# Kernel tuning notes

Measured on AMD Instinct MI355X. Metric: run time of the kernel, lower is better.

The kernel has to match this reference:

```python
import jax, jax.numpy as jnp
import numpy as np

D = 512
H = 8
DH = D // H  # 64


def setup_inputs() -> dict:
    key = jax.random.key(0)
    ks = jax.random.split(key, 7)
    batch, la, lb = 8, 256, 256
    A = jax.random.normal(ks[0], (batch, la, D), dtype=jnp.float32)
    B = jax.random.normal(ks[1], (batch, lb, D), dtype=jnp.float32)
    s = 1.0 / np.sqrt(D)
    W1 = jax.random.uniform(ks[2], (D, D), minval=-s, maxval=s, dtype=jnp.float32)
    b1 = jax.random.uniform(ks[3], (D,), minval=-s, maxval=s, dtype=jnp.float32)
    W2 = jax.random.uniform(ks[4], (D, D), minval=-s, maxval=s, dtype=jnp.float32)
    b2 = jax.random.uniform(ks[5], (D,), minval=-s, maxval=s, dtype=jnp.float32)
    q = jax.random.normal(ks[6], (DH,), dtype=jnp.float32) * 0.1
    return {"A": A, "B": B, "W1": W1, "b1": b1, "W2": W2, "b2": b2, "q": q}


def reference(A, B, W1, b1, W2, b2, q):
    bs, la, _ = A.shape
    lb = B.shape[1]
    # Linear + ReLU, then raw row-major reshape to (batch, heads, len, dh)
    # (matches torch .view semantics: NOT a head-transpose split)
    A_ = jax.nn.relu(A @ W1.T + b1).reshape(bs, H, la, DH)
    B_ = jax.nn.relu(B @ W2.T + b2).reshape(bs, H, lb, DH)
    # bilinear score: tanh of elementwise pairwise product, dotted with q
    # att_maps: [bs, H, la, lb]
    att_maps = jnp.einsum(
        "bhijc,c->bhij",
        jnp.tanh(A_[:, :, :, None, :] * B_[:, :, None, :, :]),
        q,
    )
    temp_b2a = jax.nn.softmax(jnp.mean(att_maps, axis=3), axis=2)  # [bs,H,la]
    temp_a2b = jax.nn.softmax(jnp.mean(att_maps, axis=2), axis=2)  # [bs,H,lb]
    A_heads = A.reshape(bs, H, la, DH)
    B_heads = B.reshape(bs, H, lb, DH)
    A_p = jnp.sum(A_heads * temp_b2a[..., None], axis=2).reshape(bs, -1)  # [bs, d]
    B_p = jnp.sum(B_heads * temp_a2b[..., None], axis=2).reshape(bs, -1)  # [bs, d]
    return (
        jnp.concatenate((A_p, B_p), axis=1),
        jnp.mean(temp_b2a, axis=1),
        jnp.mean(temp_a2b, axis=1),
    )
```

## Files before the change

### kernel.cpp

```cpp
#include <hip/hip_runtime.h>
#include <hip/hip_bf16.h>

#define LOG2E 1.4426950408889634f
#define SC2   2.8853900817779268f

typedef __attribute__((ext_vector_type(8))) short short8b;
typedef __attribute__((ext_vector_type(4))) short short4b;
typedef __attribute__((ext_vector_type(4))) float f32x4;

__device__ __forceinline__ float fast_exp2(float x) {
#if __has_builtin(__builtin_amdgcn_exp2f)
  return __builtin_amdgcn_exp2f(x);
#else
  return exp2f(x);
#endif
}
__device__ __forceinline__ float fast_rcp(float x) {
#if __has_builtin(__builtin_amdgcn_rcpf)
  return __builtin_amdgcn_rcpf(x);
#else
  return 1.0f / x;
#endif
}
__device__ __forceinline__ short f2bf(float f) {
  __hip_bfloat16 h = __float2bfloat16(f);
  return *reinterpret_cast<short*>(&h);
}

__global__ __launch_bounds__(256) void gemm_mfma_kernel(
    const float* __restrict__ Xa, const float* __restrict__ Wa,
    const float* __restrict__ ba, float* __restrict__ Oa,
    const float* __restrict__ Xb, const float* __restrict__ Wb,
    const float* __restrict__ bb, float* __restrict__ Ob) {
  const float* X = blockIdx.z ? Xb : Xa;
  const float* W = blockIdx.z ? Wb : Wa;
  const float* bias = blockIdx.z ? bb : ba;
  float* O = blockIdx.z ? Ob : Oa;

  __shared__ __align__(16) short As[64 * 40];
  __shared__ __align__(16) short Ws[64 * 40];

  int t = threadIdx.x;
  int m0 = blockIdx.x * 64, n0 = blockIdx.y * 64;
  int l = t & 63, w = t >> 6;
  int wm = (w >> 1) * 32, wn = (w & 1) * 32;
  int lr = l & 15, ko = (l >> 4) * 8;

  f32x4 acc[2][2];
#pragma unroll
  for (int m = 0; m < 2; ++m)
#pragma unroll
    for (int n = 0; n < 2; ++n) acc[m][n] = f32x4{0.f, 0.f, 0.f, 0.f};

  for (int k0 = 0; k0 < 512; k0 += 32) {
#pragma unroll
    for (int s = 0; s < 2; ++s) {
      int slot = t + s * 256;
      int row = slot >> 3, q = (slot & 7) << 2;
      float4 v = *reinterpret_cast<const float4*>(&X[(m0 + row) * 512 + k0 + q]);
      short4b sv = {f2bf(v.x), f2bf(v.y), f2bf(v.z), f2bf(v.w)};
      *reinterpret_cast<short4b*>(&As[row * 40 + q]) = sv;
      float4 u = *reinterpret_cast<const float4*>(&W[(n0 + row) * 512 + k0 + q]);
      short4b su = {f2bf(u.x), f2bf(u.y), f2bf(u.z), f2bf(u.w)};
      *reinterpret_cast<short4b*>(&Ws[row * 40 + q]) = su;
    }
    __syncthreads();

    short8b afr[2], bfr[2];
#pragma unroll
    for (int m = 0; m < 2; ++m)
      afr[m] = *reinterpret_cast<const short8b*>(&As[(wm + m * 16 + lr) * 40 + ko]);
#pragma unroll
    for (int n = 0; n < 2; ++n)
      bfr[n] = *reinterpret_cast<const short8b*>(&Ws[(wn + n * 16 + lr) * 40 + ko]);
#pragma unroll
    for (int m = 0; m < 2; ++m)
#pragma unroll
      for (int n = 0; n < 2; ++n)
        acc[m][n] = __builtin_amdgcn_mfma_f32_16x16x32_bf16(afr[m], bfr[n], acc[m][n], 0, 0, 0);
    __syncthreads();
  }

#pragma unroll
  for (int n = 0; n < 2; ++n) {
    int col = n0 + wn + n * 16 + lr;
    float bv = bias[col];
#pragma unroll
    for (int m = 0; m < 2; ++m) {
      int rbase = m0 + wm + m * 16 + (l >> 4) * 4;
#pragma unroll
      for (int r = 0; r < 4; ++r) {
        float v = acc[m][n][r] + bv;
        O[(rbase + r) * 512 + col] = v > 0.f ? v : 0.f;
      }
    }
  }
}

__global__ __launch_bounds__(256) void compact_kernel(
    const float* __restrict__ Br, const float* __restrict__ q,
    float2* __restrict__ Cb, unsigned* __restrict__ Cnt, float* __restrict__ Ksum) {
  int blk = blockIdx.x;
  int bh = blk >> 3, jblk = blk & 7;
  int t = threadIdx.x;
  int jl = t >> 3, p = t & 7;
  __shared__ float Bls[32][65];
  __shared__ float qls[64];

  const float* Bbase = Br + bh * 16384 + jblk * 2048;
#pragma unroll
  for (int it = 0; it < 2; ++it) {
    int idx = it * 256 + t;
    int row = idx >> 4, c4 = (idx & 15) << 2;
    float4 v = *reinterpret_cast<const float4*>(&Bbase[row * 64 + c4]);
    Bls[row][c4 + 0] = v.x; Bls[row][c4 + 1] = v.y;
    Bls[row][c4 + 2] = v.z; Bls[row][c4 + 3] = v.w;
  }
  if (t < 64) qls[t] = q[t];
  __syncthreads();

  int c0 = p * 8;
  int nz = 0;
  float K = 0.f;
#pragma unroll
  for (int cc = 0; cc < 8; ++cc) {
    float v = Bls[jl][c0 + cc];
    if (v > 0.f) { ++nz; K += qls[c0 + cc]; }
  }
  int incl = nz;
#pragma unroll
  for (int d = 1; d < 8; d <<= 1) {
    int u = __shfl_up(incl, d, 8);
    if (p >= d) incl += u;
  }
  int off = incl - nz;
  int total = __shfl(incl, 7, 8);

  float2* dst = Cb + (bh * 256 + jblk * 32 + jl) * 64;
  int k = off;
#pragma unroll
  for (int cc = 0; cc < 8; ++cc) {
    int c = c0 + cc;
    float v = Bls[jl][c];
    if (v > 0.f) {
      unsigned qb = (__float_as_uint(-2.f * qls[c]) & ~63u) | (unsigned)c;
      dst[k] = make_float2(v * SC2, __uint_as_float(qb));
      ++k;
    }
  }
#pragma unroll
  for (int d = 1; d < 8; d <<= 1) K += __shfl_xor(K, d, 8);

  if (p == 7) {
    int cnt = total;
    while (cnt & 3) { dst[cnt] = make_float2(0.f, 0.f); ++cnt; }
    Cnt[bh * 256 + jblk * 32 + jl] = (unsigned)cnt;
    Ksum[bh * 256 + jblk * 32 + jl] = K;
  }
}

__global__ __launch_bounds__(512, 8) void attmap_kernel(
    const float* __restrict__ Ar, const float2* __restrict__ Cb,
    const unsigned* __restrict__ Cnt,
    float* __restrict__ rowpart, float* __restrict__ colsum) {
  int bh = blockIdx.x, jblk = blockIdx.y, isplit = blockIdx.z;
  int t = threadIdx.x;
  int il = t & 127;
  int g = __builtin_amdgcn_readfirstlane(t >> 7);
  __shared__ __align__(16) float Als[128 * 65];
  __shared__ float red[512];
  __shared__ float cpart[8][8];

  const float* Abase = Ar + bh * 16384 + isplit * 8192;
#pragma unroll
  for (int it = 0; it < 4; ++it) {
    int idx = it * 512 + t;
    int r = idx >> 4, c4 = (idx & 15) << 2;
    float4 v = *reinterpret_cast<const float4*>(&Abase[r * 64 + c4]);
    Als[r * 65 + c4 + 0] = v.x; Als[r * 65 + c4 + 1] = v.y;
    Als[r * 65 + c4 + 2] = v.z; Als[r * 65 + c4 + 3] = v.w;
  }
  __syncthreads();

  const float* Arow = &Als[il * 65];
  float acc[8];

#pragma unroll
  for (int jj = 0; jj < 8; ++jj) {
    int jl = g * 8 + jj;
    int n = (int)__builtin_amdgcn_readfirstlane(Cnt[bh * 256 + jblk * 32 + jl]);
    const float4* P4 = reinterpret_cast<const float4*>(Cb + (bh * 256 + jblk * 32 + jl) * 64);
    float s0 = 0.f, s1 = 0.f;
    if (n > 0) {
      const int nit = n >> 2;
      float4 u0 = P4[0], v0 = P4[1];
      int i1 = (1 < nit) ? 1 : (nit - 1);
      float4 u1 = P4[i1 * 2], v1 = P4[i1 * 2 + 1];
#pragma unroll 1
      for (int it = 0; it < nit; ++it) {
        int i2 = it + 2; i2 = (i2 < nit) ? i2 : (nit - 1);
        float4 u2 = P4[i2 * 2], v2 = P4[i2 * 2 + 1];
        float g0 = Arow[__float_as_uint(u0.y) & 63u];
        float g1 = Arow[__float_as_uint(u0.w) & 63u];
        float g2 = Arow[__float_as_uint(v0.y) & 63u];
        float g3 = Arow[__float_as_uint(v0.w) & 63u];
        float e0 = fast_exp2(g0 * u0.x);
        float e1 = fast_exp2(g1 * u0.z);
        float e2 = fast_exp2(g2 * v0.x);
        float e3 = fast_exp2(g3 * v0.z);
        float w0 = e0 + 1.f, w1 = e1 + 1.f, w2 = e2 + 1.f, w3 = e3 + 1.f;
        float n01 = fmaf(u0.w, w0, u0.y * w1);
        float n23 = fmaf(v0.w, w2, v0.y * w3);
        s0 = fmaf(n01, fast_rcp(w0 * w1), s0);
        s1 = fmaf(n23, fast_rcp(w2 * w3), s1);
        u0 = u1; v0 = v1; u1 = u2; v1 = v2;
      }
    }
    acc[jj] = s0 + s1;
  }

  float rs = 0.f;
#pragma unroll
  for (int jj = 0; jj < 8; ++jj) rs += acc[jj];
  red[t] = rs;

  int lane = t & 63, w = t >> 6;
#pragma unroll
  for (int jj = 0; jj < 8; ++jj) {
    float v = acc[jj];
#pragma unroll
    for (int off = 32; off >= 1; off >>= 1) v += __shfl_xor(v, off);
    if (lane == 0) cpart[w][jj] = v;
  }
  __syncthreads();
  if (t < 128) {
    rowpart[(bh * 8 + jblk) * 256 + isplit * 128 + t] =
        red[t] + red[t + 128] + red[t + 256] + red[t + 384];
  } else if (t < 160) {
    int jl = t - 128;
    int gg = jl >> 3, jj = jl & 7;
    colsum[(bh * 2 + isplit) * 256 + jblk * 32 + jl] =
        cpart[2 * gg][jj] + cpart[2 * gg + 1][jj];
  }
}

__global__ __launch_bounds__(512) void softmax_pool_kernel(
    const float* __restrict__ rowpart, const float* __restrict__ colsum,
    const float* __restrict__ Ksum,
    const float* __restrict__ A0, const float* __restrict__ B0,
    float* __restrict__ b2a, float* __restrict__ a2b, float* __restrict__ out) {
  int bh = blockIdx.x;
  int b = bh >> 3, h = bh & 7;
  int t = threadIdx.x;
  int tt = t & 255;
  int lane = t & 63, w = (t >> 6) & 3;
  __shared__ float redA[4], redB[4], redC[4], redD[4];
  __shared__ float tA[256], tB[256];
  __shared__ float pp[8][64];

  float r = 0.f;
#pragma unroll
  for (int jb = 0; jb < 8; ++jb) r += rowpart[(bh * 8 + jb) * 256 + tt];
  r *= (1.f / 256.f);
  float cs = Ksum[bh * 256 + tt] +
             (colsum[(bh * 2 + 0) * 256 + tt] + colsum[(bh * 2 + 1) * 256 + tt]) * (1.f / 256.f);

  float mr = r, mc = cs;
#pragma unroll
  for (int off = 32; off >= 1; off >>= 1) {
    mr = fmaxf(mr, __shfl_xor(mr, off));
    mc = fmaxf(mc, __shfl_xor(mc, off));
  }
  if (lane == 0) { redA[w] = mr; redB[w] = mc; }
  __syncthreads();
  mr = fmaxf(fmaxf(redA[0], redA[1]), fmaxf(redA[2], redA[3]));
  mc = fmaxf(fmaxf(redB[0], redB[1]), fmaxf(redB[2], redB[3]));

  float er = fast_exp2((r - mr) * LOG2E);
  float ec = fast_exp2((cs - mc) * LOG2E);
  float sr = er, sc = ec;
#pragma unroll
  for (int off = 32; off >= 1; off >>= 1) {
    sr += __shfl_xor(sr, off);
    sc += __shfl_xor(sc, off);
  }
  if (lane == 0) { redC[w] = sr; redD[w] = sc; }
  __syncthreads();
  sr = redC[0] + redC[1] + redC[2] + redC[3];
  sc = redD[0] + redD[1] + redD[2] + redD[3];

  float vb2a = er * fast_rcp(sr);
  float va2b = ec * fast_rcp(sc);
  tA[tt] = vb2a; tB[tt] = va2b;
  b2a[bh * 256 + tt] = vb2a;
  a2b[bh * 256 + tt] = va2b;
  __syncthreads();

  int c = t & 63, iq = t >> 6;
  const float* Ab = A0 + b * 131072 + h * 16384;
  const float* Bb = B0 + b * 131072 + h * 16384;
  float pa = 0.f, pb = 0.f;
#pragma unroll 4
  for (int ii = 0; ii < 32; ++ii) {
    int i = (iq << 5) + ii;
    pa = fmaf(Ab[i * 64 + c], tA[i], pa);
    pb = fmaf(Bb[i * 64 + c], tB[i], pb);
  }
  pp[iq][c] = pa;
  __syncthreads();
  if (t < 64) {
    float s = 0.f;
#pragma unroll
    for (int k = 0; k < 8; ++k) s += pp[k][t];
    out[b * 1024 + h * 64 + t] = s;
  }
  __syncthreads();
  pp[iq][c] = pb;
  __syncthreads();
  if (t < 64) {
    float s = 0.f;
#pragma unroll
    for (int k = 0; k < 8; ++k) s += pp[k][t];
    out[b * 1024 + 512 + h * 64 + t] = s;
  }
}

__global__ __launch_bounds__(256) void mean_heads_kernel(
    const float* __restrict__ b2a, const float* __restrict__ a2b,
    float* __restrict__ out) {
  int b = blockIdx.x, t = threadIdx.x;
  float s1 = 0.f, s2 = 0.f;
#pragma unroll
  for (int h = 0; h < 8; ++h) {
    s1 += b2a[(b * 8 + h) * 256 + t];
    s2 += a2b[(b * 8 + h) * 256 + t];
  }
  out[8192 + b * 256 + t] = s1 * 0.125f;
  out[10240 + b * 256 + t] = s2 * 0.125f;
}

extern "C" void kernel_launch(void* const* d_in, const int* in_sizes, int n_in,
                              void* d_out, int out_size, void* d_ws, size_t ws_size,
                              hipStream_t stream) {
  const float* A  = (const float*)d_in[0];
  const float* B  = (const float*)d_in[1];
  const float* W1 = (const float*)d_in[2];
  const float* b1 = (const float*)d_in[3];
  const float* W2 = (const float*)d_in[4];
  const float* b2 = (const float*)d_in[5];
  const float* q  = (const float*)d_in[6];
  float* out = (float*)d_out;
  float* ws = (float*)d_ws;

  float*    Ar      = ws;
  float*    Brr     = ws + 1048576;
  float2*   Cb      = (float2*)(ws + 2097152);
  unsigned* Cnt     = (unsigned*)(ws + 4194304);
  float*    Ksum    = ws + 4210688;
  float*    rowpart = ws + 4227072;
  float*    colsum  = ws + 4358144;
  float*    b2a     = ws;
  float*    a2b     = ws + 16384;

  gemm_mfma_kernel<<<dim3(32, 8, 2), 256, 0, stream>>>(A, W1, b1, Ar, B, W2, b2, Brr);
  compact_kernel<<<512, 256, 0, stream>>>(Brr, q, Cb, Cnt, Ksum);
  attmap_kernel<<<dim3(64, 8, 2), 512, 0, stream>>>(Ar, Cb, Cnt, rowpart, colsum);
  softmax_pool_kernel<<<64, 512, 0, stream>>>(rowpart, colsum, Ksum, A, B, b2a, a2b, out);
  mean_heads_kernel<<<8, 256, 0, stream>>>(b2a, a2b, out);
}
```

Baseline: 68.54 us.

## Fuse B compaction into GEMM epilogue and split pooling across chunks

```diff
diff --git a/kernel.cpp b/kernel.cpp
--- a/kernel.cpp
+++ b/kernel.cpp
@@ -27,18 +27,22 @@
   return *reinterpret_cast<short*>(&h);
 }
 
-__global__ __launch_bounds__(256) void gemm_mfma_kernel(
+__global__ __launch_bounds__(256) void gemm_fused_kernel(
     const float* __restrict__ Xa, const float* __restrict__ Wa,
     const float* __restrict__ ba, float* __restrict__ Oa,
     const float* __restrict__ Xb, const float* __restrict__ Wb,
-    const float* __restrict__ bb, float* __restrict__ Ob) {
-  const float* X = blockIdx.z ? Xb : Xa;
-  const float* W = blockIdx.z ? Wb : Wa;
-  const float* bias = blockIdx.z ? bb : ba;
-  float* O = blockIdx.z ? Ob : Oa;
+    const float* __restrict__ bb, const float* __restrict__ q,
+    float2* __restrict__ Cb, unsigned* __restrict__ Cnt,
+    float* __restrict__ Ksum) {
+  const int isB = blockIdx.z;
+  const float* X = isB ? Xb : Xa;
+  const float* W = isB ? Wb : Wa;
+  const float* bias = isB ? bb : ba;
 
   __shared__ __align__(16) short As[64 * 40];
   __shared__ __align__(16) short Ws[64 * 40];
+  __shared__ __align__(16) float Btile[64][65];
+  __shared__ float qls[64];
 
   int t = threadIdx.x;
   int m0 = blockIdx.x * 64, n0 = blockIdx.y * 64;
@@ -46,6 +50,8 @@
   int wm = (w >> 1) * 32, wn = (w & 1) * 32;
   int lr = l & 15, ko = (l >> 4) * 8;
 
+  if (isB && t < 64) qls[t] = q[t];
+
   f32x4 acc[2][2];
 #pragma unroll
   for (int m = 0; m < 2; ++m)
@@ -56,13 +62,13 @@
 #pragma unroll
     for (int s = 0; s < 2; ++s) {
       int slot = t + s * 256;
-      int row = slot >> 3, q = (slot & 7) << 2;
-      float4 v = *reinterpret_cast<const float4*>(&X[(m0 + row) * 512 + k0 + q]);
+      int row = slot >> 3, qd = (slot & 7) << 2;
+      float4 v = *reinterpret_cast<const float4*>(&X[(m0 + row) * 512 + k0 + qd]);
       short4b sv = {f2bf(v.x), f2bf(v.y), f2bf(v.z), f2bf(v.w)};
-      *reinterpret_cast<short4b*>(&As[row * 40 + q]) = sv;
-      float4 u = *reinterpret_cast<const float4*>(&W[(n0 + row) * 512 + k0 + q]);
+      *reinterpret_cast<short4b*>(&As[row * 40 + qd]) = sv;
+      float4 u = *reinterpret_cast<const float4*>(&W[(n0 + row) * 512 + k0 + qd]);
       short4b su = {f2bf(u.x), f2bf(u.y), f2bf(u.z), f2bf(u.w)};
-      *reinterpret_cast<short4b*>(&Ws[row * 40 + q]) = su;
+      *reinterpret_cast<short4b*>(&Ws[row * 40 + qd]) = su;
     }
     __syncthreads();
 
@@ -81,81 +87,81 @@
     __syncthreads();
   }
 
+  if (!isB) {
+#pragma unroll
+    for (int n = 0; n < 2; ++n) {
+      int col = n0 + wn + n * 16 + lr;
+      float bv = bias[col];
+#pragma unroll
+      for (int m = 0; m < 2; ++m) {
+        int rbase = m0 + wm + m * 16 + (l >> 4) * 4;
+#pragma unroll
+        for (int r = 0; r < 4; ++r) {
+          float v = acc[m][n][r] + bv;
+          Oa[(rbase + r) * 512 + col] = v > 0.f ? v : 0.f;
+        }
+      }
+    }
+    return;
+  }
+
 #pragma unroll
   for (int n = 0; n < 2; ++n) {
-    int col = n0 + wn + n * 16 + lr;
-    float bv = bias[col];
+    int col = wn + n * 16 + lr;
+    float bv = bias[n0 + col];
 #pragma unroll
     for (int m = 0; m < 2; ++m) {
-      int rbase = m0 + wm + m * 16 + (l >> 4) * 4;
+      int rbase = wm + m * 16 + (l >> 4) * 4;
 #pragma unroll
       for (int r = 0; r < 4; ++r) {
         float v = acc[m][n][r] + bv;
-        O[(rbase + r) * 512 + col] = v > 0.f ? v : 0.f;
+        Btile[rbase + r][col] = v > 0.f ? v : 0.f;
       }
     }
   }
-}
-
-__global__ __launch_bounds__(256) void compact_kernel(
-    const float* __restrict__ Br, const float* __restrict__ q,
-    float2* __restrict__ Cb, unsigned* __restrict__ Cnt, float* __restrict__ Ksum) {
-  int blk = blockIdx.x;
-  int bh = blk >> 3, jblk = blk & 7;
-  int t = threadIdx.x;
-  int jl = t >> 3, p = t & 7;
-  __shared__ float Bls[32][65];
-  __shared__ float qls[64];
-
-  const float* Bbase = Br + bh * 16384 + jblk * 2048;
-#pragma unroll
-  for (int it = 0; it < 2; ++it) {
-    int idx = it * 256 + t;
-    int row = idx >> 4, c4 = (idx & 15) << 2;
-    float4 v = *reinterpret_cast<const float4*>(&Bbase[row * 64 + c4]);
-    Bls[row][c4 + 0] = v.x; Bls[row][c4 + 1] = v.y;
-    Bls[row][c4 + 2] = v.z; Bls[row][c4 + 3] = v.w;
-  }
-  if (t < 64) qls[t] = q[t];
-  __syncthreads();
-
-  int c0 = p * 8;
+  __syncthreads();
+
+  int jl = t >> 2, p = t & 3;
+  int row = m0 + jl;
+  int bh = (row >> 8) * 8 + ((row >> 5) & 7);
+  int j = ((row & 31) << 3) + (n0 >> 6);
+  int c0 = p * 16;
+
   int nz = 0;
   float K = 0.f;
 #pragma unroll
-  for (int cc = 0; cc < 8; ++cc) {
-    float v = Bls[jl][c0 + cc];
+  for (int cc = 0; cc < 16; ++cc) {
+    float v = Btile[jl][c0 + cc];
     if (v > 0.f) { ++nz; K += qls[c0 + cc]; }
   }
   int incl = nz;
 #pragma unroll
-  for (int d = 1; d < 8; d <<= 1) {
-    int u = __shfl_up(incl, d, 8);
+  for (int d = 1; d < 4; d <<= 1) {
+    int u = __shfl_up(incl, d, 4);
     if (p >= d) incl += u;
   }
   int off = incl - nz;
-  int total = __shfl(incl, 7, 8);
-
-  float2* dst = Cb + (bh * 256 + jblk * 32 + jl) * 64;
+  int total = __shfl(incl, 3, 4);
+
+  float2* dst = Cb + (bh * 256 + j) * 64;
   int k = off;
 #pragma unroll
-  for (int cc = 0; cc < 8; ++cc) {
+  for (int cc = 0; cc < 16; ++cc) {
     int c = c0 + cc;
-    float v = Bls[jl][c];
+    float v = Btile[jl][c];
     if (v > 0.f) {
       unsigned qb = (__float_as_uint(-2.f * qls[c]) & ~63u) | (unsigned)c;
       dst[k] = make_float2(v * SC2, __uint_as_float(qb));
       ++k;
     }
   }
-#pragma unroll
-  for (int d = 1; d < 8; d <<= 1) K += __shfl_xor(K, d, 8);
-
-  if (p == 7) {
+  K += __shfl_xor(K, 1, 4);
+  K += __shfl_xor(K, 2, 4);
+  if (p == 3) {
     int cnt = total;
     while (cnt & 3) { dst[cnt] = make_float2(0.f, 0.f); ++cnt; }
-    Cnt[bh * 256 + jblk * 32 + jl] = (unsigned)cnt;
-    Ksum[bh * 256 + jblk * 32 + jl] = K;
+    Cnt[bh * 256 + j] = (unsigned)cnt;
+    Ksum[bh * 256 + j] = K;
   }
 }
 
@@ -248,8 +254,9 @@
     const float* __restrict__ rowpart, const float* __restrict__ colsum,
     const float* __restrict__ Ksum,
     const float* __restrict__ A0, const float* __restrict__ B0,
-    float* __restrict__ b2a, float* __restrict__ a2b, float* __restrict__ out) {
-  int bh = blockIdx.x;
+    float* __restrict__ b2a, float* __restrict__ a2b,
+    float* __restrict__ poolA, float* __restrict__ poolB) {
+  int bh = blockIdx.x, chunk = blockIdx.y;
   int b = bh >> 3, h = bh & 7;
   int t = threadIdx.x;
   int tt = t & 255;
@@ -292,40 +299,43 @@
   float vb2a = er * fast_rcp(sr);
   float va2b = ec * fast_rcp(sc);
   tA[tt] = vb2a; tB[tt] = va2b;
-  b2a[bh * 256 + tt] = vb2a;
-  a2b[bh * 256 + tt] = va2b;
-  __syncthreads();
-
-  int c = t & 63, iq = t >> 6;
+  if (chunk == 0) {
+    b2a[bh * 256 + tt] = vb2a;
+    a2b[bh * 256 + tt] = va2b;
+  }
+  __syncthreads();
+
+  int c = t & 63, isub = t >> 6;
   const float* Ab = A0 + b * 131072 + h * 16384;
   const float* Bb = B0 + b * 131072 + h * 16384;
   float pa = 0.f, pb = 0.f;
-#pragma unroll 4
-  for (int ii = 0; ii < 32; ++ii) {
-    int i = (iq << 5) + ii;
+#pragma unroll
+  for (int ii = 0; ii < 8; ++ii) {
+    int i = chunk * 64 + isub * 8 + ii;
     pa = fmaf(Ab[i * 64 + c], tA[i], pa);
     pb = fmaf(Bb[i * 64 + c], tB[i], pb);
   }
-  pp[iq][c] = pa;
+  pp[isub][c] = pa;
   __syncthreads();
   if (t < 64) {
     float s = 0.f;
 #pragma unroll
     for (int k = 0; k < 8; ++k) s += pp[k][t];
-    out[b * 1024 + h * 64 + t] = s;
-  }
-  __syncthreads();
-  pp[iq][c] = pb;
+    poolA[(bh * 4 + chunk) * 64 + t] = s;
+  }
+  __syncthreads();
+  pp[isub][c] = pb;
   __syncthreads();
   if (t < 64) {
     float s = 0.f;
 #pragma unroll
     for (int k = 0; k < 8; ++k) s += pp[k][t];
-    out[b * 1024 + 512 + h * 64 + t] = s;
-  }
-}
-
-__global__ __launch_bounds__(256) void mean_heads_kernel(
+    poolB[(bh * 4 + chunk) * 64 + t] = s;
+  }
+}
+
+__global__ __launch_bounds__(256) void final_kernel(
+    const float* __restrict__ poolA, const float* __restrict__ poolB,
     const float* __restrict__ b2a, const float* __restrict__ a2b,
     float* __restrict__ out) {
   int b = blockIdx.x, t = threadIdx.x;
@@ -337,6 +347,17 @@
   }
   out[8192 + b * 256 + t] = s1 * 0.125f;
   out[10240 + b * 256 + t] = s2 * 0.125f;
+
+#pragma unroll
+  for (int hh = 0; hh < 2; ++hh) {
+    int idx = hh * 256 + t;
+    int h = idx >> 6, c = idx & 63;
+    int base = ((b * 8 + h) * 4) * 64 + c;
+    float sA = poolA[base] + poolA[base + 64] + poolA[base + 128] + poolA[base + 192];
+    float sB = poolB[base] + poolB[base + 64] + poolB[base + 128] + poolB[base + 192];
+    out[b * 1024 + h * 64 + c] = sA;
+    out[b * 1024 + 512 + h * 64 + c] = sB;
+  }
 }
 
 extern "C" void kernel_launch(void* const* d_in, const int* in_sizes, int n_in,
@@ -353,18 +374,20 @@
   float* ws = (float*)d_ws;
 
   float*    Ar      = ws;
-  float*    Brr     = ws + 1048576;
-  float2*   Cb      = (float2*)(ws + 2097152);
-  unsigned* Cnt     = (unsigned*)(ws + 4194304);
-  float*    Ksum    = ws + 4210688;
-  float*    rowpart = ws + 4227072;
-  float*    colsum  = ws + 4358144;
-  float*    b2a     = ws;
-  float*    a2b     = ws + 16384;
-
-  gemm_mfma_kernel<<<dim3(32, 8, 2), 256, 0, stream>>>(A, W1, b1, Ar, B, W2, b2, Brr);
-  compact_kernel<<<512, 256, 0, stream>>>(Brr, q, Cb, Cnt, Ksum);
+  float2*   Cb      = (float2*)(ws + 1048576);
+  unsigned* Cnt     = (unsigned*)(ws + 3145728);
+  float*    Ksum    = ws + 3162112;
+  float*    rowpart = ws + 3178496;
+  float*    colsum  = ws + 3309568;
+  float*    b2a     = ws + 3342336;
+  float*    a2b     = ws + 3358720;
+  float*    poolA   = ws + 3375104;
+  float*    poolB   = ws + 3391488;
+
+  gemm_fused_kernel<<<dim3(32, 8, 2), 256, 0, stream>>>(
+      A, W1, b1, Ar, B, W2, b2, q, Cb, Cnt, Ksum);
   attmap_kernel<<<dim3(64, 8, 2), 512, 0, stream>>>(Ar, Cb, Cnt, rowpart, colsum);
-  softmax_pool_kernel<<<64, 512, 0, stream>>>(rowpart, colsum, Ksum, A, B, b2a, a2b, out);
-  mean_heads_kernel<<<8, 256, 0, stream>>>(b2a, a2b, out);
-}
+  softmax_pool_kernel<<<dim3(64, 4), 512, 0, stream>>>(
+      rowpart, colsum, Ksum, A, B, b2a, a2b, poolA, poolB);
+  final_kernel<<<8, 256, 0, stream>>>(poolA, poolB, b2a, a2b, out);
+}
```

After: 64.45 us (median of 2 runs). 1.06x faster.
